# Performance work log

Hardware: AMD Instinct MI355X
Metric: run time of the kernel (lower is better)

Reference implementation:

```python
import jax, jax.numpy as jnp
import numpy as np

V, E, HID, T = 50000, 512, 1024, 16   # vocab, embed_dim, hidden_dim, tagset
H = HID // 2                          # per-direction LSTM hidden
B, S = 32, 512                        # batch, seq_len
NEG = -10000.0                        # start/stop transitions are set to -10000 in __init__


def setup_inputs() -> dict:
    key = jax.random.key(0)
    ks = jax.random.split(key, 12)
    g = lambda i, shape, scale: (jax.random.normal(ks[i], shape, jnp.float32) * scale)
    return {
        "sentence": jax.random.randint(ks[0], (B, S), 0, V),
        "embedding": g(1, (V, E), 1.0),
        # PyTorch LSTM gate order i,f,g,o; bias fused (b_ih + b_hh)
        "Wih_f": g(2, (4 * H, E), 0.04), "Whh_f": g(3, (4 * H, H), 0.04), "b_f": g(4, (4 * H,), 0.04),
        "Wih_b": g(5, (4 * H, E), 0.04), "Whh_b": g(6, (4 * H, H), 0.04), "b_b": g(7, (4 * H,), 0.04),
        "W_out": g(8, (T, HID), 0.04), "b_out": g(9, (T,), 0.04),
        "transitions": g(10, (T, T), 0.35),   # xavier_normal-ish
        "start_trans": jnp.full((T,), NEG, jnp.float32),
        "stop_trans": jnp.full((T,), NEG, jnp.float32),
    }


def _lstm_dir(x, Wih, Whh, b, reverse):
    # x: [B, S, E] -> h sequence [B, S, H]
    bsz, hid = x.shape[0], Whh.shape[1]

    def step(carry, xt):
        h, c = carry
        gates = xt @ Wih.T + h @ Whh.T + b          # [B, 4H]
        i, f, gg, o = jnp.split(gates, 4, axis=-1)
        c = jax.nn.sigmoid(f) * c + jax.nn.sigmoid(i) * jnp.tanh(gg)
        h = jax.nn.sigmoid(o) * jnp.tanh(c)
        return (h, c), h

    init = (jnp.zeros((bsz, hid), x.dtype), jnp.zeros((bsz, hid), x.dtype))
    _, hs = jax.lax.scan(step, init, jnp.swapaxes(x, 0, 1), reverse=reverse)
    return jnp.swapaxes(hs, 0, 1)


def _features(sentence, embedding, Wih_f, Whh_f, b_f, Wih_b, Whh_b, b_b, W_out, b_out):
    emb = embedding[sentence]                                  # [B, S, E]
    hf = _lstm_dir(emb, Wih_f, Whh_f, b_f, reverse=False)      # [B, S, H]
    hb = _lstm_dir(emb, Wih_b, Whh_b, b_b, reverse=True)       # [B, S, H]
    return jnp.concatenate([hf, hb], -1) @ W_out.T + b_out     # [B, S, T]


def reference(sentence, embedding, Wih_f, Whh_f, b_f, Wih_b, Whh_b, b_b,
              W_out, b_out, transitions, start_trans, stop_trans):
    feats = _features(sentence, embedding, Wih_f, Whh_f, b_f,
                      Wih_b, Whh_b, b_b, W_out, b_out)         # [B, S, T]

    # ---- Viterbi DP (forward pass with backpointers) ----
    v0 = feats[:, 0] + start_trans                             # [B, T]

    def step(v, feat):
        scores = v[:, :, None] + transitions[None]             # [B, Tprev, Tcur]
        idx = jnp.argmax(scores, axis=1)                       # [B, T] backpointers
        v = jnp.max(scores, axis=1) + feat
        return v, idx

    v, idxs = jax.lax.scan(step, v0, jnp.swapaxes(feats[:, 1:], 0, 1))  # idxs: [S-1, B, T]
    last = jnp.argmax(v + stop_trans, axis=-1)                 # [B]

    # ---- backtrace ----
    def back(tag, idx):
        prev = jnp.take_along_axis(idx, tag[:, None], axis=1)[:, 0]
        return prev, prev

    _, prevs = jax.lax.scan(back, last, idxs, reverse=True)    # [S-1, B]
    tags = jnp.concatenate([jnp.swapaxes(prevs, 0, 1), last[:, None]], axis=1)  # [B, S]
    return tags
```

## Files before the change

kernel.cpp:

```cpp
#include <hip/hip_runtime.h>
#include <stdint.h>

#define BATCH 32
#define SEQ   512
#define EDIM  512
#define HID   512
#define NG    2048
#define NTAG  16

typedef _Float16 f16;
typedef _Float16 f16x4 __attribute__((ext_vector_type(4)));
typedef _Float16 f16x8 __attribute__((ext_vector_type(8)));
typedef float    f32x4 __attribute__((ext_vector_type(4)));

#define LO_SCALE 2048.0f
#define LO_INV   (1.0f/2048.0f)

__global__ __launch_bounds__(256) void k_split(const float* __restrict__ src,
                                               f16* __restrict__ hi, f16* __restrict__ lo, int n) {
    int i = blockIdx.x * blockDim.x + threadIdx.x;
    int stride = gridDim.x * blockDim.x;
    for (; i < n; i += stride) {
        float x = src[i];
        f16 h = (f16)x;
        hi[i] = h;
        lo[i] = (f16)((x - (float)h) * LO_SCALE);
    }
}

__global__ __launch_bounds__(256) void k_gather(const int* __restrict__ sent,
                                                const float* __restrict__ emb,
                                                f16* __restrict__ ehi, f16* __restrict__ elo) {
    int m = blockIdx.x;
    int idx = sent[m];
    const float* src = emb + (size_t)idx * EDIM;
    int k = threadIdx.x * 2;
    float2 v = *(const float2*)(src + k);
    f16 h0 = (f16)v.x, h1 = (f16)v.y;
    ehi[(size_t)m*EDIM + k]     = h0;
    ehi[(size_t)m*EDIM + k + 1] = h1;
    elo[(size_t)m*EDIM + k]     = (f16)((v.x - (float)h0) * LO_SCALE);
    elo[(size_t)m*EDIM + k + 1] = (f16)((v.y - (float)h1) * LO_SCALE);
}

__device__ __forceinline__ void gld16(const void* g, void* l) {
    __builtin_amdgcn_global_load_lds((const __attribute__((address_space(1))) uint32_t*)g,
                                     (__attribute__((address_space(3))) uint32_t*)l, 16, 0, 0);
}
__device__ __forceinline__ f32x4 mfma16(f16x8 a, f16x8 b, f32x4 c) {
    return __builtin_amdgcn_mfma_f32_16x16x32_f16(a, b, c, 0, 0, 0);
}

__global__ __launch_bounds__(512, 2) void k_gemm(
    const f16* __restrict__ Ahi, const f16* __restrict__ Alo,
    const f16* __restrict__ Whi, const f16* __restrict__ Wlo,
    const float* __restrict__ bias_f, const float* __restrict__ bias_b,
    float* __restrict__ Xout)
{
    const int n0  = blockIdx.x * 128;
    const int m0  = blockIdx.y * 128;
    const int dir = blockIdx.z;
    const float* bias = dir ? bias_b : bias_f;
    const f16* Bhi = Whi + (size_t)dir * NG * EDIM;
    const f16* Blo = Wlo + (size_t)dir * NG * EDIM;
    float* X = Xout + (size_t)dir * 16384 * NG;

    __shared__ f16 sAh[128*64], sAl[128*64], sBh[128*64], sBl[128*64];

    const int tid  = threadIdx.x;
    const int lane = tid & 63;
    const int wave = tid >> 6;
    const int wr   = wave >> 2;
    const int wc   = wave & 3;

    f32x4 accH[4][2] = {};
    f32x4 accM[4][2] = {};

    for (int kt = 0; kt < 8; ++kt) {
        const int kbase = kt * 64;
        for (int sub = 0; sub < 2; ++sub) {
            int byte = sub*8192 + tid*16;
            int row  = byte >> 7;
            int up   = (byte >> 4) & 7;
            int u    = up ^ (row & 7);
            const f16* ga  = Ahi + (size_t)(m0 + row)*EDIM + kbase + u*8;
            const f16* gal = Alo + (size_t)(m0 + row)*EDIM + kbase + u*8;
            const f16* gb  = Bhi + (size_t)(n0 + row)*EDIM + kbase + u*8;
            const f16* gbl = Blo + (size_t)(n0 + row)*EDIM + kbase + u*8;
            gld16(ga,  (char*)sAh + byte);
            gld16(gal, (char*)sAl + byte);
            gld16(gb,  (char*)sBh + byte);
            gld16(gbl, (char*)sBl + byte);
        }
        __syncthreads();
        for (int ks = 0; ks < 2; ++ks) {
            f16x8 fAh[4], fAl[4], fBh[2], fBl[2];
            #pragma unroll
            for (int mi = 0; mi < 4; ++mi) {
                int row = wr*64 + mi*16 + (lane & 15);
                int u   = ks*4 + (lane >> 4);
                int off = row*128 + (u ^ (row & 7))*16;
                fAh[mi] = *(const f16x8*)((const char*)sAh + off);
                fAl[mi] = *(const f16x8*)((const char*)sAl + off);
            }
            #pragma unroll
            for (int ni = 0; ni < 2; ++ni) {
                int row = wc*32 + ni*16 + (lane & 15);
                int u   = ks*4 + (lane >> 4);
                int off = row*128 + (u ^ (row & 7))*16;
                fBh[ni] = *(const f16x8*)((const char*)sBh + off);
                fBl[ni] = *(const f16x8*)((const char*)sBl + off);
            }
            #pragma unroll
            for (int mi = 0; mi < 4; ++mi)
                #pragma unroll
                for (int ni = 0; ni < 2; ++ni)
                    accH[mi][ni] = mfma16(fAh[mi], fBh[ni], accH[mi][ni]);
            #pragma unroll
            for (int mi = 0; mi < 4; ++mi)
                #pragma unroll
                for (int ni = 0; ni < 2; ++ni)
                    accM[mi][ni] = mfma16(fAh[mi], fBl[ni], accM[mi][ni]);
            #pragma unroll
            for (int mi = 0; mi < 4; ++mi)
                #pragma unroll
                for (int ni = 0; ni < 2; ++ni)
                    accM[mi][ni] = mfma16(fAl[mi], fBh[ni], accM[mi][ni]);
        }
        __syncthreads();
    }
    #pragma unroll
    for (int ni = 0; ni < 2; ++ni) {
        int col = n0 + wc*32 + ni*16 + (lane & 15);
        float bv = bias[col];
        int gate  = col >> 9;
        int chunk = (col >> 4) & 31;
        int u     = col & 15;
        #pragma unroll
        for (int mi = 0; mi < 4; ++mi) {
            #pragma unroll
            for (int j = 0; j < 4; ++j) {
                int m = m0 + wr*64 + mi*16 + (lane >> 4)*4 + j;
                int b = m >> 9, s = m & 511;
                X[(((size_t)chunk*32 + b)*512 + s)*64 + gate*16 + u] =
                    accH[mi][ni][j] + accM[mi][ni][j]*LO_INV + bv;
            }
        }
    }
}

__global__ __launch_bounds__(512, 1) void k_rec(
    const float* __restrict__ Xall,
    const f16* __restrict__ Whi, const f16* __restrict__ Wlo,
    unsigned* __restrict__ hx,
    float* __restrict__ h_hist)
{
    __shared__ char  hhiS[16384];
    __shared__ char  hloS[16384];
    __shared__ float gbuf[2*4*16*17];

    const int wg    = blockIdx.x;
    const int dir   = wg >> 6;
    const int mt    = (wg >> 5) & 1;
    const int chunk = wg & 31;
    const int u0    = chunk * 16;
    const int tid   = threadIdx.x;
    const int lane  = tid & 63;
    const int wave  = tid >> 6;
    const int g     = wave & 3;
    const int kh    = wave >> 2;
    const int u     = lane & 15;
    const int q4    = lane >> 4;

    const float* X = Xall + (size_t)dir * 16384 * NG;
    unsigned* hxd = hx + (size_t)dir * 2 * BATCH * HID;

    const int pbl = tid >> 4;
    const int pu  = tid & 15;
    const char* hrowH = hhiS + u*1024;
    const char* hrowL = hloS + u*1024;
    const int u7 = u & 7;

    f16x8 bhv[8], blv[8];
    {
        const size_t row = (size_t)(dir*NG + g*512 + u0 + u) * EDIM;
        const f16* ph = Whi + row + q4*8;
        const f16* pl = Wlo + row + q4*8;
        #pragma unroll
        for (int kt = 0; kt < 8; ++kt) {
            bhv[kt] = *(const f16x8*)(ph + (kh*8 + kt)*32);
            blv[kt] = *(const f16x8*)(pl + (kh*8 + kt)*32);
        }
    }

    float c = 0.0f;

    for (int t = 0; t < SEQ; ++t) {
        const int s = dir ? (SEQ - 1 - t) : t;

        float xv[4];
        {
            const float* xb = X + (((size_t)chunk*32 + (mt*16 + pbl))*512 + s)*64 + pu;
            #pragma unroll
            for (int gg = 0; gg < 4; ++gg) xv[gg] = xb[gg*16];
        }

        if (t == 0) {
            #pragma unroll
            for (int i = 0; i < 4; ++i) {
                int q = i*512 + tid, row = q >> 7, kq = (q & 127)*4;
                int off = row*1024 + ((kq >> 3) ^ (row & 7))*16 + (kq & 4)*2;
                *(uint2*)(hhiS + off) = (uint2){0u, 0u};
                *(uint2*)(hloS + off) = (uint2){0u, 0u};
            }
        } else {
            const unsigned tag32 = ((unsigned)((t - 1) >> 1) & 3u) << 16;
            const unsigned* hsrc = hxd + (size_t)(t & 1)*BATCH*HID + (size_t)mt*16*HID;
            unsigned pend = 0xFu;
            while (pend) {
                unsigned long long va[4], vb[4];
                #pragma unroll
                for (int i = 0; i < 4; ++i) {
                    if (pend & (1u << i)) {
                        int q = i*512 + tid;
                        const unsigned long long* p =
                            (const unsigned long long*)(hsrc + (q >> 7)*HID + (q & 127)*4);
                        va[i] = __hip_atomic_load(p,     __ATOMIC_RELAXED, __HIP_MEMORY_SCOPE_AGENT);
                        vb[i] = __hip_atomic_load(p + 1, __ATOMIC_RELAXED, __HIP_MEMORY_SCOPE_AGENT);
                    }
                }
                #pragma unroll
                for (int i = 0; i < 4; ++i) {
                    if (!(pend & (1u << i))) continue;
                    unsigned w0 = (unsigned)va[i], w1 = (unsigned)(va[i] >> 32);
                    unsigned w2 = (unsigned)vb[i], w3 = (unsigned)(vb[i] >> 32);
                    if ((((w0 ^ tag32) | (w1 ^ tag32) | (w2 ^ tag32) | (w3 ^ tag32)) & 0x30000u) != 0u)
                        continue;
                    unsigned hi01 = (w0 & 0xffffu) | (w1 << 16);
                    unsigned hi23 = (w2 & 0xffffu) | (w3 << 16);
                    unsigned lo01 = (w0 >> 16) | (w1 & 0xffff0000u);
                    unsigned lo23 = (w2 >> 16) | (w3 & 0xffff0000u);
                    int q = i*512 + tid, row = q >> 7, kq = (q & 127)*4;
                    int off = row*1024 + ((kq >> 3) ^ (row & 7))*16 + (kq & 4)*2;
                    *(uint2*)(hhiS + off) = (uint2){hi01, hi23};
                    *(uint2*)(hloS + off) = (uint2){lo01, lo23};
                    pend &= ~(1u << i);
                }
            }
        }
        __syncthreads();

        f32x4 aH = {0.f,0.f,0.f,0.f}, aM1 = aH, aM2 = aH;
        #pragma unroll
        for (int kt = 0; kt < 8; ++kt) {
            int ug = (kh*8 + kt)*4 + q4;
            f16x8 ah = *(const f16x8*)(hrowH + (ug ^ u7)*16);
            f16x8 al = *(const f16x8*)(hrowL + (ug ^ u7)*16);
            aH  = mfma16(ah, bhv[kt], aH);
            aM1 = mfma16(ah, blv[kt], aM1);
            aM2 = mfma16(al, bhv[kt], aM2);
        }
        #pragma unroll
        for (int j = 0; j < 4; ++j) {
            int row = q4*4 + j;
            gbuf[(kh*4 + g)*272 + row*17 + u] = aH[j] + (aM1[j] + aM2[j]) * LO_INV;
        }
        __syncthreads();

        if (tid < 256) {
            float gs[4];
            #pragma unroll
            for (int gg = 0; gg < 4; ++gg)
                gs[gg] = gbuf[(0*4 + gg)*272 + pbl*17 + pu]
                       + gbuf[(1*4 + gg)*272 + pbl*17 + pu] + xv[gg];
            float si = 1.0f / (1.0f + __expf(-gs[0]));
            float sf = 1.0f / (1.0f + __expf(-gs[1]));
            float tg = 1.0f - 2.0f / (__expf(2.0f*gs[2]) + 1.0f);
            float so = 1.0f / (1.0f + __expf(-gs[3]));
            c = sf * c + si * tg;
            float hval = so * (1.0f - 2.0f / (__expf(2.0f*c) + 1.0f));
            f16 hh = (f16)hval;
            f16 hl = (f16)((hval - (float)hh) * LO_SCALE);
            unsigned packed = (unsigned)__builtin_bit_cast(unsigned short, hh)
                            | ((unsigned)__builtin_bit_cast(unsigned short, hl) << 16);
            packed = (packed & ~0x30000u) | ((((unsigned)t >> 1) & 3u) << 16);
            int b = mt*16 + pbl;
            unsigned* hdst = hxd + (size_t)((t + 1) & 1)*BATCH*HID + b*HID + u0 + pu;
            __hip_atomic_store(hdst, packed, __ATOMIC_RELAXED, __HIP_MEMORY_SCOPE_AGENT);
            __builtin_nontemporal_store(hval,
                h_hist + ((size_t)b*SEQ + s)*1024 + dir*HID + u0 + pu);
        }
    }
}

__global__ __launch_bounds__(256) void k_feats(
    const float* __restrict__ H,
    const float* __restrict__ Wout,
    const float* __restrict__ bout,
    float* __restrict__ feats)
{
    __shared__ float Wt[1024][16];
    int tid = threadIdx.x;
    for (int i = tid; i < 16384; i += 256)
        Wt[i >> 4][i & 15] = Wout[(i & 15)*1024 + (i >> 4)];
    __syncthreads();
    int wave = tid >> 6, lane = tid & 63;
    int row = blockIdx.x * 4 + wave;
    const float* hrow = H + (size_t)row * 1024;
    float acc[16];
    #pragma unroll
    for (int t = 0; t < 16; ++t) acc[t] = 0.f;
    #pragma unroll
    for (int cc = 0; cc < 4; ++cc) {
        float4 hv = *(const float4*)(hrow + cc*256 + lane*4);
        #pragma unroll
        for (int j = 0; j < 4; ++j) {
            int k = cc*256 + lane*4 + j;
            float h = (&hv.x)[j];
            #pragma unroll
            for (int tg = 0; tg < 16; ++tg) acc[tg] += h * Wt[k][tg];
        }
    }
    #pragma unroll
    for (int off = 32; off >= 1; off >>= 1) {
        #pragma unroll
        for (int tg = 0; tg < 16; ++tg) acc[tg] += __shfl_xor(acc[tg], off);
    }
    if (lane == 0) {
        #pragma unroll
        for (int tg = 0; tg < 16; ++tg)
            feats[(size_t)row*16 + tg] = acc[tg] + bout[tg];
    }
}

__global__ __launch_bounds__(64) void k_viterbi(
    const float* __restrict__ feats,
    const float* __restrict__ trans,
    const float* __restrict__ startt, const float* __restrict__ stopt,
    int* __restrict__ out)
{
    __shared__ unsigned char bp[511*16];
    int b = blockIdx.x;
    int lane = threadIdx.x;
    int cur = lane & 15;
    int q   = lane >> 4;
    float tr[4];
    #pragma unroll
    for (int i = 0; i < 4; ++i) tr[i] = trans[(q*4 + i)*16 + cur];
    const float* fb = feats + (size_t)b * SEQ * NTAG;
    float v = fb[cur] + startt[cur];
    for (int s = 1; s < SEQ; ++s) {
        float best = -1e30f; int bi = 0;
        #pragma unroll
        for (int i = 0; i < 4; ++i) {
            float pv = __shfl(v, q*4 + i);
            float sc = pv + tr[i];
            if (sc > best) { best = sc; bi = q*4 + i; }
        }
        #pragma unroll
        for (int off = 16; off <= 32; off <<= 1) {
            float ob = __shfl_xor(best, off);
            int   oi = __shfl_xor(bi, off);
            if (ob > best || (ob == best && oi < bi)) { best = ob; bi = oi; }
        }
        if (lane < 16) bp[(s - 1)*16 + cur] = (unsigned char)bi;
        v = best + fb[s*16 + cur];
    }
    float sc = v + stopt[cur];
    int bc = cur;
    #pragma unroll
    for (int off = 1; off <= 32; off <<= 1) {
        float os = __shfl_xor(sc, off);
        int   oc = __shfl_xor(bc, off);
        if (os > sc || (os == sc && oc < bc)) { sc = os; bc = oc; }
    }
    __syncthreads();
    if (lane == 0) {
        int curt = bc;
        out[b*SEQ + SEQ - 1] = curt;
        for (int s2 = SEQ - 2; s2 >= 0; --s2) {
            curt = bp[s2*16 + curt];
            out[b*SEQ + s2] = curt;
        }
    }
}

extern "C" void kernel_launch(void* const* d_in, const int* in_sizes, int n_in,
                              void* d_out, int out_size, void* d_ws, size_t ws_size,
                              hipStream_t stream) {
    (void)in_sizes; (void)n_in; (void)out_size; (void)ws_size;
    const int*   sentence  = (const int*)  d_in[0];
    const float* embedding = (const float*)d_in[1];
    const float* Wih_f = (const float*)d_in[2];
    const float* Whh_f = (const float*)d_in[3];
    const float* b_f   = (const float*)d_in[4];
    const float* Wih_b = (const float*)d_in[5];
    const float* Whh_b = (const float*)d_in[6];
    const float* b_b   = (const float*)d_in[7];
    const float* W_out = (const float*)d_in[8];
    const float* b_out = (const float*)d_in[9];
    const float* trans = (const float*)d_in[10];
    const float* startt= (const float*)d_in[11];
    const float* stopt = (const float*)d_in[12];

    char* ws = (char*)d_ws;
    float* X      = (float*)(ws);
    float* h_hist = (float*)(ws + 268435456ull);
    f16*   ehi    = (f16*)  (ws + 335544320ull);
    f16*   elo    = (f16*)  (ws + 352321536ull);
    f16*   wihhi  = (f16*)  (ws + 369098752ull);
    f16*   wihlo  = (f16*)  (ws + 373293056ull);
    f16*   whhhi  = (f16*)  (ws + 377487360ull);
    f16*   whhlo  = (f16*)  (ws + 381681664ull);
    unsigned* hx  = (unsigned*)(ws + 385875968ull);
    float* feats  = (float*)(ws + 386138112ull);

    hipMemsetAsync(hx, 0xFF, 262144, stream);

    k_split<<<1024, 256, 0, stream>>>(Wih_f, wihhi,          wihlo,          NG*EDIM);
    k_split<<<1024, 256, 0, stream>>>(Wih_b, wihhi + NG*EDIM, wihlo + NG*EDIM, NG*EDIM);
    k_split<<<1024, 256, 0, stream>>>(Whh_f, whhhi,          whhlo,          NG*EDIM);
    k_split<<<1024, 256, 0, stream>>>(Whh_b, whhhi + NG*EDIM, whhlo + NG*EDIM, NG*EDIM);
    k_gather<<<16384, 256, 0, stream>>>(sentence, embedding, ehi, elo);

    k_gemm<<<dim3(16, 128, 2), 512, 0, stream>>>(ehi, elo, wihhi, wihlo, b_f, b_b, X);

    k_rec<<<128, 512, 0, stream>>>(X, whhhi, whhlo, hx, h_hist);

    k_feats<<<4096, 256, 0, stream>>>(h_hist, W_out, b_out, feats);
    k_viterbi<<<32, 64, 0, stream>>>(feats, trans, startt, stopt, (int*)d_out);
}
```

Before: 2.364 ms.

## Fuse input projection GEMM into recurrent LSTM kernel

Removes the separate input-to-hidden GEMM kernel and its large fp32 gate buffer. Each timestep the recurrent kernel now loads the embedding rows into LDS and runs the Wih MFMAs alongside the Whh MFMAs, keeping Wih slices in registers and adding the bias directly. This drops the X write and read traffic and one launch, but doubles the MFMA work and register use on the serial critical path of the recurrence.

```diff
diff --git a/kernel.cpp b/kernel.cpp
--- a/kernel.cpp
+++ b/kernel.cpp
@@ -51,112 +51,18 @@
     return __builtin_amdgcn_mfma_f32_16x16x32_f16(a, b, c, 0, 0, 0);
 }
 
-__global__ __launch_bounds__(512, 2) void k_gemm(
-    const f16* __restrict__ Ahi, const f16* __restrict__ Alo,
-    const f16* __restrict__ Whi, const f16* __restrict__ Wlo,
-    const float* __restrict__ bias_f, const float* __restrict__ bias_b,
-    float* __restrict__ Xout)
-{
-    const int n0  = blockIdx.x * 128;
-    const int m0  = blockIdx.y * 128;
-    const int dir = blockIdx.z;
-    const float* bias = dir ? bias_b : bias_f;
-    const f16* Bhi = Whi + (size_t)dir * NG * EDIM;
-    const f16* Blo = Wlo + (size_t)dir * NG * EDIM;
-    float* X = Xout + (size_t)dir * 16384 * NG;
-
-    __shared__ f16 sAh[128*64], sAl[128*64], sBh[128*64], sBl[128*64];
-
-    const int tid  = threadIdx.x;
-    const int lane = tid & 63;
-    const int wave = tid >> 6;
-    const int wr   = wave >> 2;
-    const int wc   = wave & 3;
-
-    f32x4 accH[4][2] = {};
-    f32x4 accM[4][2] = {};
-
-    for (int kt = 0; kt < 8; ++kt) {
-        const int kbase = kt * 64;
-        for (int sub = 0; sub < 2; ++sub) {
-            int byte = sub*8192 + tid*16;
-            int row  = byte >> 7;
-            int up   = (byte >> 4) & 7;
-            int u    = up ^ (row & 7);
-            const f16* ga  = Ahi + (size_t)(m0 + row)*EDIM + kbase + u*8;
-            const f16* gal = Alo + (size_t)(m0 + row)*EDIM + kbase + u*8;
-            const f16* gb  = Bhi + (size_t)(n0 + row)*EDIM + kbase + u*8;
-            const f16* gbl = Blo + (size_t)(n0 + row)*EDIM + kbase + u*8;
-            gld16(ga,  (char*)sAh + byte);
-            gld16(gal, (char*)sAl + byte);
-            gld16(gb,  (char*)sBh + byte);
-            gld16(gbl, (char*)sBl + byte);
-        }
-        __syncthreads();
-        for (int ks = 0; ks < 2; ++ks) {
-            f16x8 fAh[4], fAl[4], fBh[2], fBl[2];
-            #pragma unroll
-            for (int mi = 0; mi < 4; ++mi) {
-                int row = wr*64 + mi*16 + (lane & 15);
-                int u   = ks*4 + (lane >> 4);
-                int off = row*128 + (u ^ (row & 7))*16;
-                fAh[mi] = *(const f16x8*)((const char*)sAh + off);
-                fAl[mi] = *(const f16x8*)((const char*)sAl + off);
-            }
-            #pragma unroll
-            for (int ni = 0; ni < 2; ++ni) {
-                int row = wc*32 + ni*16 + (lane & 15);
-                int u   = ks*4 + (lane >> 4);
-                int off = row*128 + (u ^ (row & 7))*16;
-                fBh[ni] = *(const f16x8*)((const char*)sBh + off);
-                fBl[ni] = *(const f16x8*)((const char*)sBl + off);
-            }
-            #pragma unroll
-            for (int mi = 0; mi < 4; ++mi)
-                #pragma unroll
-                for (int ni = 0; ni < 2; ++ni)
-                    accH[mi][ni] = mfma16(fAh[mi], fBh[ni], accH[mi][ni]);
-            #pragma unroll
-            for (int mi = 0; mi < 4; ++mi)
-                #pragma unroll
-                for (int ni = 0; ni < 2; ++ni)
-                    accM[mi][ni] = mfma16(fAh[mi], fBl[ni], accM[mi][ni]);
-            #pragma unroll
-            for (int mi = 0; mi < 4; ++mi)
-                #pragma unroll
-                for (int ni = 0; ni < 2; ++ni)
-                    accM[mi][ni] = mfma16(fAl[mi], fBh[ni], accM[mi][ni]);
-        }
-        __syncthreads();
-    }
-    #pragma unroll
-    for (int ni = 0; ni < 2; ++ni) {
-        int col = n0 + wc*32 + ni*16 + (lane & 15);
-        float bv = bias[col];
-        int gate  = col >> 9;
-        int chunk = (col >> 4) & 31;
-        int u     = col & 15;
-        #pragma unroll
-        for (int mi = 0; mi < 4; ++mi) {
-            #pragma unroll
-            for (int j = 0; j < 4; ++j) {
-                int m = m0 + wr*64 + mi*16 + (lane >> 4)*4 + j;
-                int b = m >> 9, s = m & 511;
-                X[(((size_t)chunk*32 + b)*512 + s)*64 + gate*16 + u] =
-                    accH[mi][ni][j] + accM[mi][ni][j]*LO_INV + bv;
-            }
-        }
-    }
-}
-
 __global__ __launch_bounds__(512, 1) void k_rec(
-    const float* __restrict__ Xall,
-    const f16* __restrict__ Whi, const f16* __restrict__ Wlo,
+    const f16* __restrict__ ehi,  const f16* __restrict__ elo,
+    const f16* __restrict__ Whhi, const f16* __restrict__ Whlo,
+    const f16* __restrict__ Wihi, const f16* __restrict__ Wilo,
+    const float* __restrict__ b_f, const float* __restrict__ b_b,
     unsigned* __restrict__ hx,
     float* __restrict__ h_hist)
 {
     __shared__ char  hhiS[16384];
     __shared__ char  hloS[16384];
+    __shared__ char  ehiS[16384];
+    __shared__ char  eloS[16384];
     __shared__ float gbuf[2*4*16*17];
 
     const int wg    = blockIdx.x;
@@ -172,37 +78,54 @@
     const int u     = lane & 15;
     const int q4    = lane >> 4;
 
-    const float* X = Xall + (size_t)dir * 16384 * NG;
     unsigned* hxd = hx + (size_t)dir * 2 * BATCH * HID;
 
     const int pbl = tid >> 4;
     const int pu  = tid & 15;
     const char* hrowH = hhiS + u*1024;
     const char* hrowL = hloS + u*1024;
+    const char* erowH = ehiS + u*1024;
+    const char* erowL = eloS + u*1024;
     const int u7 = u & 7;
 
-    f16x8 bhv[8], blv[8];
+    f16x8 bhv[8], blv[8], wbh[8], wbl[8];
     {
         const size_t row = (size_t)(dir*NG + g*512 + u0 + u) * EDIM;
-        const f16* ph = Whi + row + q4*8;
-        const f16* pl = Wlo + row + q4*8;
+        const f16* ph = Whhi + row + q4*8;
+        const f16* pl = Whlo + row + q4*8;
+        const f16* qh = Wihi + row + q4*8;
+        const f16* ql = Wilo + row + q4*8;
         #pragma unroll
         for (int kt = 0; kt < 8; ++kt) {
             bhv[kt] = *(const f16x8*)(ph + (kh*8 + kt)*32);
             blv[kt] = *(const f16x8*)(pl + (kh*8 + kt)*32);
-        }
-    }
+            wbh[kt] = *(const f16x8*)(qh + (kh*8 + kt)*32);
+            wbl[kt] = *(const f16x8*)(ql + (kh*8 + kt)*32);
+        }
+    }
+
+    float bv[4];
+    {
+        const float* bias = dir ? b_b : b_f;
+        #pragma unroll
+        for (int gg = 0; gg < 4; ++gg) bv[gg] = bias[gg*512 + u0 + pu];
+    }
+
+    const int grow0 = mt*16 + wave;
+    const int srcu  = (lane ^ wave) * 8;
 
     float c = 0.0f;
 
     for (int t = 0; t < SEQ; ++t) {
         const int s = dir ? (SEQ - 1 - t) : t;
 
-        float xv[4];
         {
-            const float* xb = X + (((size_t)chunk*32 + (mt*16 + pbl))*512 + s)*64 + pu;
-            #pragma unroll
-            for (int gg = 0; gg < 4; ++gg) xv[gg] = xb[gg*16];
+            size_t r0 = ((size_t)(grow0)*SEQ + s) * EDIM + srcu;
+            size_t r1 = ((size_t)(grow0 + 8)*SEQ + s) * EDIM + srcu;
+            gld16(ehi + r0, ehiS + tid*16);
+            gld16(ehi + r1, ehiS + 8192 + tid*16);
+            gld16(elo + r0, eloS + tid*16);
+            gld16(elo + r1, eloS + 8192 + tid*16);
         }
 
         if (t == 0) {
@@ -253,9 +176,14 @@
         f32x4 aH = {0.f,0.f,0.f,0.f}, aM1 = aH, aM2 = aH;
         #pragma unroll
         for (int kt = 0; kt < 8; ++kt) {
-            int ug = (kh*8 + kt)*4 + q4;
-            f16x8 ah = *(const f16x8*)(hrowH + (ug ^ u7)*16);
-            f16x8 al = *(const f16x8*)(hrowL + (ug ^ u7)*16);
+            int off = (((kh*8 + kt)*4 + q4) ^ u7) * 16;
+            f16x8 eh = *(const f16x8*)(erowH + off);
+            f16x8 el = *(const f16x8*)(erowL + off);
+            f16x8 ah = *(const f16x8*)(hrowH + off);
+            f16x8 al = *(const f16x8*)(hrowL + off);
+            aH  = mfma16(eh, wbh[kt], aH);
+            aM1 = mfma16(eh, wbl[kt], aM1);
+            aM2 = mfma16(el, wbh[kt], aM2);
             aH  = mfma16(ah, bhv[kt], aH);
             aM1 = mfma16(ah, blv[kt], aM1);
             aM2 = mfma16(al, bhv[kt], aM2);
@@ -272,7 +200,7 @@
             #pragma unroll
             for (int gg = 0; gg < 4; ++gg)
                 gs[gg] = gbuf[(0*4 + gg)*272 + pbl*17 + pu]
-                       + gbuf[(1*4 + gg)*272 + pbl*17 + pu] + xv[gg];
+                       + gbuf[(1*4 + gg)*272 + pbl*17 + pu] + bv[gg];
             float si = 1.0f / (1.0f + __expf(-gs[0]));
             float sf = 1.0f / (1.0f + __expf(-gs[1]));
             float tg = 1.0f - 2.0f / (__expf(2.0f*gs[2]) + 1.0f);
@@ -404,16 +332,15 @@
     const float* stopt = (const float*)d_in[12];
 
     char* ws = (char*)d_ws;
-    float* X      = (float*)(ws);
-    float* h_hist = (float*)(ws + 268435456ull);
-    f16*   ehi    = (f16*)  (ws + 335544320ull);
-    f16*   elo    = (f16*)  (ws + 352321536ull);
-    f16*   wihhi  = (f16*)  (ws + 369098752ull);
-    f16*   wihlo  = (f16*)  (ws + 373293056ull);
-    f16*   whhhi  = (f16*)  (ws + 377487360ull);
-    f16*   whhlo  = (f16*)  (ws + 381681664ull);
-    unsigned* hx  = (unsigned*)(ws + 385875968ull);
-    float* feats  = (float*)(ws + 386138112ull);
+    float* h_hist = (float*)(ws);
+    f16*   ehi    = (f16*)  (ws +  67108864ull);
+    f16*   elo    = (f16*)  (ws +  83886080ull);
+    f16*   wihhi  = (f16*)  (ws + 100663296ull);
+    f16*   wihlo  = (f16*)  (ws + 104857600ull);
+    f16*   whhhi  = (f16*)  (ws + 109051904ull);
+    f16*   whhlo  = (f16*)  (ws + 113246208ull);
+    unsigned* hx  = (unsigned*)(ws + 117440512ull);
+    float* feats  = (float*)(ws + 117702656ull);
 
     hipMemsetAsync(hx, 0xFF, 262144, stream);
 
@@ -423,9 +350,8 @@
     k_split<<<1024, 256, 0, stream>>>(Whh_b, whhhi + NG*EDIM, whhlo + NG*EDIM, NG*EDIM);
     k_gather<<<16384, 256, 0, stream>>>(sentence, embedding, ehi, elo);
 
-    k_gemm<<<dim3(16, 128, 2), 512, 0, stream>>>(ehi, elo, wihhi, wihlo, b_f, b_b, X);
-
-    k_rec<<<128, 512, 0, stream>>>(X, whhhi, whhlo, hx, h_hist);
+    k_rec<<<128, 512, 0, stream>>>(ehi, elo, whhhi, whhlo, wihhi, wihlo,
+                                   b_f, b_b, hx, h_hist);
 
     k_feats<<<4096, 256, 0, stream>>>(h_hist, W_out, b_out, feats);
     k_viterbi<<<32, 64, 0, stream>>>(feats, trans, startt, stopt, (int*)d_out);
```

After: 2.291 ms. 3.1% less time.
